# Optimization experiments

Hardware: AMD Instinct MI355X
Metric: run time of the kernel (lower is better)

## Reference

```python
import jax, jax.numpy as jnp
import numpy as np

B, S, D, H, E = 2, 2048, 1024, 4096, 8


def setup_inputs() -> dict:
    key = jax.random.key(0)
    ks = jax.random.split(key, 8)
    sc = lambda *shape: 0.02
    x = jax.random.normal(ks[0], (B, S, D), dtype=jnp.float32)
    gate_w = jax.random.normal(ks[1], (D, E), dtype=jnp.float32) * 0.02
    gate_b = jnp.zeros((E,), dtype=jnp.float32)
    w1 = jax.random.normal(ks[2], (E, D, H), dtype=jnp.float32) * 0.02
    b1 = jnp.zeros((E, H), dtype=jnp.float32)
    w2 = jax.random.normal(ks[3], (E, H, D), dtype=jnp.float32) * 0.02
    b2 = jnp.zeros((E, D), dtype=jnp.float32)
    return {"x": x, "gate_w": gate_w, "gate_b": gate_b,
            "w1": w1, "b1": b1, "w2": w2, "b2": b2}


def reference(x, gate_w, gate_b, w1, b1, w2, b2):
    b, s, d = x.shape
    e = w1.shape[0]
    xf = x.reshape(-1, d)                       # [N, D]
    scores = xf @ gate_w + gate_b               # [N, E]
    # original does topk(k=2) but only uses topk_indices[:, 0] == argmax
    sel = jnp.argmax(scores, axis=-1)           # [N]
    out = jnp.zeros_like(xf)
    for ei in range(e):                         # small fixed expert loop
        h = jax.nn.gelu(xf @ w1[ei] + b1[ei], approximate=False)
        y = h @ w2[ei] + b2[ei]
        out = out + jnp.where((sel == ei)[:, None], y, jnp.zeros((), x.dtype))
    out = out.reshape(b, s, d)
    l_aux = jnp.zeros((), dtype=x.dtype)
    return out, l_aux
```

## Files before the change

kernel.cpp:

```cpp
#include <hip/hip_runtime.h>
#include <math.h>

#define NTOK 4096
#define DDIM 1024
#define HDIM 4096
#define NEXP 8
#define BK 64
#define T0MAX 40
#define T1MAX 72
#define NG0 ((HDIM / 128) * T0MAX)
#define NCVT2 ((DDIM / 64) * (NEXP * (HDIM / 64)))

typedef float f32x4 __attribute__((ext_vector_type(4)));
typedef __bf16 bf16x8 __attribute__((ext_vector_type(8)));
typedef const __attribute__((address_space(1))) void gas_t;
typedef __attribute__((address_space(3))) void las_t;

__device__ __forceinline__ unsigned short f2bf(float f) {
    union { float f; unsigned u; } v; v.f = f;
    unsigned u = v.u;
    return (unsigned short)((u + 0x7fffu + ((u >> 16) & 1u)) >> 16);
}

__device__ __forceinline__ float gelu_f(float v) {
    return 0.5f * v * (1.0f + erff(v * 0.70710678118654752f));
}

__global__ void k_gate(const float* __restrict__ x, const float* __restrict__ gw,
                       const float* __restrict__ gb, unsigned short* __restrict__ xb,
                       int* __restrict__ sel, int* __restrict__ counts) {
    const int wid = threadIdx.x >> 6, lane = threadIdx.x & 63;
    const int tok = blockIdx.x * 4 + wid;
    const float4* xr4 = (const float4*)(x + (long)tok * DDIM);
    unsigned short* xbr = xb + (long)tok * DDIM;
    float s[NEXP];
#pragma unroll
    for (int e = 0; e < NEXP; ++e) s[e] = 0.f;
#pragma unroll
    for (int it = 0; it < DDIM / 256; ++it) {
        const int q = it * 64 + lane;
        const float4 xv = xr4[q];
        *(ushort4*)(xbr + q * 4) = make_ushort4(f2bf(xv.x), f2bf(xv.y), f2bf(xv.z), f2bf(xv.w));
#pragma unroll
        for (int j = 0; j < 4; ++j) {
            const float xs = (j == 0) ? xv.x : (j == 1) ? xv.y : (j == 2) ? xv.z : xv.w;
            const float4* g4 = (const float4*)(gw + (long)(q * 4 + j) * NEXP);
            const float4 g0 = g4[0], g1 = g4[1];
            s[0] += xs * g0.x; s[1] += xs * g0.y; s[2] += xs * g0.z; s[3] += xs * g0.w;
            s[4] += xs * g1.x; s[5] += xs * g1.y; s[6] += xs * g1.z; s[7] += xs * g1.w;
        }
    }
#pragma unroll
    for (int e = 0; e < NEXP; ++e)
        for (int off = 32; off > 0; off >>= 1)
            s[e] += __shfl_down(s[e], off);
    if (lane == 0) {
        float best = s[0] + gb[0]; int bi = 0;
#pragma unroll
        for (int e = 1; e < NEXP; ++e) {
            const float v = s[e] + gb[e];
            if (v > best) { best = v; bi = e; }
        }
        sel[tok] = bi;
        atomicAdd(&counts[bi], 1);
    }
}

__global__ void k_fill(const int* __restrict__ sel, const int* __restrict__ counts,
                       int* __restrict__ cur, int* __restrict__ offs,
                       int* __restrict__ list, int* __restrict__ t0,
                       int* __restrict__ t1, float* __restrict__ laux) {
    const int t = blockIdx.x * blockDim.x + threadIdx.x;
    if (t < NTOK) {
        const int e = sel[t];
        int off_e = 0;
#pragma unroll
        for (int j = 0; j < NEXP; ++j) off_e += (j < e) ? counts[j] : 0;
        list[off_e + atomicAdd(&cur[e], 1)] = t;
    }
    if (t == 0) {
        int o = 0;
        for (int e = 0; e < NEXP; ++e) { offs[e] = o; o += counts[e]; }
        offs[NEXP] = o;
        int i0 = 0;
        for (int e = 0; e < NEXP; ++e)
            for (int m = 0; m < counts[e]; m += 128) t0[i0++] = (e << 16) | m;
        while (i0 < T0MAX) t0[i0++] = -1;
        int i1 = 0;
        for (int e = 0; e < NEXP; ++e)
            for (int m = 0; m < counts[e]; m += 64) t1[i1++] = (e << 16) | m;
        while (i1 < T1MAX) t1[i1++] = -1;
        laux[0] = 0.f;
    }
}

template<int K, int NC>
__device__ __forceinline__ void cvt_tile(const float* __restrict__ W,
                                         unsigned short* __restrict__ Wt,
                                         int bx, int by, unsigned short* T) {
    constexpr int ktiles = K / 64;
    const int e  = by / ktiles;
    const int k0 = (by % ktiles) * 64;
    const int n0 = bx * 64;
    const float* src = W + (long)e * K * NC + (long)k0 * NC + n0;
    const int tid = threadIdx.x;
#pragma unroll
    for (int i = 0; i < 4; ++i) {
        const int idx = tid + i * 256;
        const int k = idx >> 4, c4 = (idx & 15) * 4;
        const float4 v = *(const float4*)(src + (long)k * NC + c4);
        T[(c4 + 0) * 68 + k] = f2bf(v.x);
        T[(c4 + 1) * 68 + k] = f2bf(v.y);
        T[(c4 + 2) * 68 + k] = f2bf(v.z);
        T[(c4 + 3) * 68 + k] = f2bf(v.w);
    }
    __syncthreads();
    unsigned short* dst = Wt + (long)e * NC * K + (long)n0 * K + k0;
#pragma unroll
    for (int i = 0; i < 2; ++i) {
        const int idx = tid + i * 256;
        const int n = idx >> 3, c8 = (idx & 7) * 8;
        *(ushort4*)(dst + (long)n * K + c8)     = *(const ushort4*)&T[n * 68 + c8];
        *(ushort4*)(dst + (long)n * K + c8 + 4) = *(const ushort4*)&T[n * 68 + c8 + 4];
    }
}

template<int K, int NC>
__global__ __launch_bounds__(256) void k_cvt_w(const float* __restrict__ W,
                                               unsigned short* __restrict__ Wt) {
    __shared__ unsigned short T[64 * 68];
    cvt_tile<K, NC>(W, Wt, blockIdx.x, blockIdx.y, T);
}

template<int MODE, int BM_, int BN_, bool FUSE>
__global__ __launch_bounds__(256) void k_gemm(
        const unsigned short* __restrict__ Ain,
        const unsigned short* __restrict__ Wt,
        const float* __restrict__ bias,
        unsigned short* __restrict__ Hout, float* __restrict__ Yout,
        const int* __restrict__ counts, const int* __restrict__ offs,
        const int* __restrict__ list, const int* __restrict__ ttab,
        const float* __restrict__ Wcvt, unsigned short* __restrict__ Wtcvt) {
    static_assert(BM_ % 32 == 0 && BN_ % 32 == 0, "tile");
    constexpr int K    = (MODE == 0) ? DDIM : HDIM;
    constexpr int NC   = (MODE == 0) ? HDIM : DDIM;
    constexpr int NT   = K / BK;
    constexpr int FM   = BM_ / 32;
    constexpr int FN   = BN_ / 32;
    constexpr int LA   = BM_ / 32;
    constexpr int LB   = BN_ / 32;
    constexpr int HALF = BM_ * 64 + BN_ * 64;
    constexpr int EP   = 136;
    constexpr int SH_SZ = (2 * HALF > BM_ * EP) ? 2 * HALF : BM_ * EP;

    __shared__ __align__(16) unsigned short sh[SH_SZ];

    int bx, by;
    if constexpr (FUSE) {
        const int bid = blockIdx.x;
        if (bid >= NG0) {
            const int cv = bid - NG0;
            cvt_tile<HDIM, DDIM>(Wcvt, Wtcvt, cv % (DDIM / 64), cv / (DDIM / 64), sh);
            return;
        }
        bx = bid % (NC / BN_); by = bid / (NC / BN_);
    } else {
        bx = blockIdx.x; by = blockIdx.y;
    }

    const int code = ttab[by];
    if (code < 0) return;
    const int e  = code >> 16;
    const int m0 = code & 0xFFFF;
    const int cnt  = counts[e];
    const int base = offs[e];
    const int n0   = bx * BN_;

    const int tid  = threadIdx.x;
    const int lane = tid & 63, wid = tid >> 6;
    const int lr = lane >> 3, lc = lane & 7;
    const int sb = (lc * 16) ^ (lr << 4);

    const unsigned short* pA[LA];
#pragma unroll
    for (int i = 0; i < LA; ++i) {
        const int r = wid * (BM_ / 4) + i * 8 + lr;
        int rr = m0 + r; if (rr >= cnt) rr = cnt - 1;
        const long grow = (MODE == 0) ? (long)list[base + rr] : (long)(base + rr);
        pA[i] = (const unsigned short*)((const char*)(Ain + grow * K) + sb);
    }
    const unsigned short* We = Wt + (long)e * NC * K;
    const unsigned short* pB[LB];
#pragma unroll
    for (int i = 0; i < LB; ++i) {
        const int r = wid * (BN_ / 4) + i * 8 + lr;
        pB[i] = (const unsigned short*)((const char*)(We + (long)(n0 + r) * K) + sb);
    }

    const int wm = (wid >> 1) * (BM_ / 2);
    const int wn = (wid & 1) * (BN_ / 2);
    const int hk = 16 * (lane >> 4);

#define STAGE(t) do { if ((t) < NT) {                                                    \
    unsigned short* Ad = sh + ((t) & 1) * HALF + (wid * (BM_ / 4)) * 64;                 \
    unsigned short* Bd = sh + ((t) & 1) * HALF + BM_ * 64 + (wid * (BN_ / 4)) * 64;      \
    _Pragma("unroll") for (int i = 0; i < LA; ++i)                                       \
        __builtin_amdgcn_global_load_lds((gas_t*)(pA[i] + (t) * 64),                     \
            (las_t*)(Ad + i * 512), 16, 0, 0);                                           \
    _Pragma("unroll") for (int i = 0; i < LB; ++i)                                       \
        __builtin_amdgcn_global_load_lds((gas_t*)(pB[i] + (t) * 64),                     \
            (las_t*)(Bd + i * 512), 16, 0, 0); } } while (0)

    const f32x4 zero4 = {0.f, 0.f, 0.f, 0.f};
    f32x4 acc[FM][FN];
#pragma unroll
    for (int i = 0; i < FM; ++i)
#pragma unroll
        for (int j = 0; j < FN; ++j) acc[i][j] = zero4;

    STAGE(0);
    STAGE(1);

    for (int t = 0; t < NT; ++t) {
        const unsigned short* Ab = sh + (t & 1) * HALF;
        const unsigned short* Bb = Ab + BM_ * 64;
        if (t + 1 < NT) { asm volatile("s_waitcnt vmcnt(%0)" :: "n"(LA + LB) : "memory"); }
        else            { asm volatile("s_waitcnt vmcnt(0)" ::: "memory"); }
        __builtin_amdgcn_sched_barrier(0);
        __builtin_amdgcn_s_barrier();
        __builtin_amdgcn_sched_barrier(0);
#pragma unroll
        for (int kk = 0; kk < BK; kk += 32) {
            bf16x8 a[FM], b[FN];
#pragma unroll
            for (int mf = 0; mf < FM; ++mf) {
                const int r  = wm + mf * 16 + (lane & 15);
                const int kb = (2 * kk + hk) ^ ((r & 7) << 4);
                a[mf] = *(const bf16x8*)((const char*)Ab + r * 128 + kb);
            }
#pragma unroll
            for (int nf = 0; nf < FN; ++nf) {
                const int cc = wn + nf * 16 + (lane & 15);
                const int kb = (2 * kk + hk) ^ ((cc & 7) << 4);
                b[nf] = *(const bf16x8*)((const char*)Bb + cc * 128 + kb);
            }
            __builtin_amdgcn_s_setprio(1);
#pragma unroll
            for (int mf = 0; mf < FM; ++mf)
#pragma unroll
                for (int nf = 0; nf < FN; ++nf)
                    acc[mf][nf] = __builtin_amdgcn_mfma_f32_16x16x32_bf16(
                        a[mf], b[nf], acc[mf][nf], 0, 0, 0);
            __builtin_amdgcn_s_setprio(0);
        }
        __builtin_amdgcn_sched_barrier(0);
        __builtin_amdgcn_s_barrier();
        __builtin_amdgcn_sched_barrier(0);
        STAGE(t + 2);
    }
#undef STAGE

    if constexpr (MODE == 0) {
#pragma unroll
        for (int nf = 0; nf < FN; ++nf) {
            const int cl = wn + nf * 16 + (lane & 15);
            const float bv = bias[(long)e * NC + n0 + cl];
#pragma unroll
            for (int mf = 0; mf < FM; ++mf) {
#pragma unroll
                for (int ri = 0; ri < 4; ++ri) {
                    const int rl = wm + mf * 16 + (lane >> 4) * 4 + ri;
                    sh[rl * EP + cl] = f2bf(gelu_f(acc[mf][nf][ri] + bv));
                }
            }
        }
        __syncthreads();
        const int row = tid >> 1, ch = (tid & 1) * 64;
        if (m0 + row < cnt) {
            char* dst = (char*)(Hout + (long)(base + m0 + row) * HDIM + n0 + ch);
            const char* srcp = (const char*)sh + row * (EP * 2) + ch * 2;
#pragma unroll
            for (int j = 0; j < 4; ++j) {
                const int4 v0 = *(const int4*)(srcp + j * 32);
                const int4 v1 = *(const int4*)(srcp + j * 32 + 16);
                *(int4*)(dst + j * 32)      = v0;
                *(int4*)(dst + j * 32 + 16) = v1;
            }
        }
    } else {
#pragma unroll
        for (int nf = 0; nf < FN; ++nf) {
            const int coln = n0 + wn + nf * 16 + (lane & 15);
            const float bv = bias[(long)e * NC + coln];
#pragma unroll
            for (int mf = 0; mf < FM; ++mf) {
                const int rb = m0 + wm + mf * 16 + (lane >> 4) * 4;
#pragma unroll
                for (int ri = 0; ri < 4; ++ri) {
                    const int row = rb + ri;
                    if (row < cnt)
                        Yout[(long)list[base + row] * DDIM + coln] = acc[mf][nf][ri] + bv;
                }
            }
        }
    }
}

extern "C" void kernel_launch(void* const* d_in, const int* in_sizes, int n_in,
                              void* d_out, int out_size, void* d_ws, size_t ws_size,
                              hipStream_t stream) {
    const float* x      = (const float*)d_in[0];
    const float* gate_w = (const float*)d_in[1];
    const float* gate_b = (const float*)d_in[2];
    const float* w1     = (const float*)d_in[3];
    const float* b1     = (const float*)d_in[4];
    const float* w2     = (const float*)d_in[5];
    const float* b2     = (const float*)d_in[6];
    float* out = (float*)d_out;

    char* ws = (char*)d_ws;
    int* counts  = (int*)(ws);
    int* cur     = (int*)(ws + 128);
    int* offs    = (int*)(ws + 256);
    int* t0      = (int*)(ws + 512);
    int* t1      = (int*)(ws + 768);
    int* sel     = (int*)(ws + 4096);
    int* list    = (int*)(ws + 20480);
    unsigned short* xb  = (unsigned short*)(ws + 65536);
    unsigned short* Hws = (unsigned short*)(ws + 65536 + 8388608);
    unsigned short* W1t = (unsigned short*)(ws + 65536 + 8388608 + 33554432);
    unsigned short* W2s = W1t + (size_t)NEXP * HDIM * DDIM;
    const size_t WS_SMALL = 65536 + 8388608 + 33554432 + 67108864;
    const size_t WS_BIG   = WS_SMALL + 67108864;
    if (ws_size < WS_SMALL) return;
    const bool big = ws_size >= WS_BIG;
    unsigned short* W2t = big ? W2s : W1t;

    hipMemsetAsync(ws, 0, 256, stream);
    k_gate<<<NTOK / 4, 256, 0, stream>>>(x, gate_w, gate_b, xb, sel, counts);
    k_fill<<<(NTOK + 255) / 256, 256, 0, stream>>>(sel, counts, cur, offs, list, t0, t1,
                                                   out + (long)NTOK * DDIM);

    k_cvt_w<DDIM, HDIM><<<dim3(HDIM / 64, NEXP * (DDIM / 64)), 256, 0, stream>>>(w1, W1t);

    if (big) {
        k_gemm<0, 128, 128, true><<<NG0 + NCVT2, 256, 0, stream>>>(
            xb, W1t, b1, Hws, nullptr, counts, offs, list, t0, w2, W2t);
    } else {
        k_gemm<0, 128, 128, false><<<dim3(HDIM / 128, T0MAX), 256, 0, stream>>>(
            xb, W1t, b1, Hws, nullptr, counts, offs, list, t0, nullptr, nullptr);
        k_cvt_w<HDIM, DDIM><<<dim3(DDIM / 64, NEXP * (HDIM / 64)), 256, 0, stream>>>(w2, W2t);
    }

    k_gemm<1, 64, 64, false><<<dim3(DDIM / 64, T1MAX), 256, 0, stream>>>(
        Hws, W2t, b2, nullptr, out, counts, offs, list, t1, nullptr, nullptr);
}
```

Before: 279.2 us.

## Fuse gate with W1 conversion, single-buffer GEMM staging, widen second GEMM tile

Folds the w1 fp32-to-bf16 transpose into the gating kernel as extra blocks, so one launch is removed and the conversion runs alongside gating. The GEMM's double-buffered async LDS prefetch is replaced by a single buffer with a load and two barriers every K step, which halves shared memory but stops global loads from overlapping with MFMA work. The second GEMM moves from 64x64 to 64x128 tiles, halving its grid. Exposed load latency in both GEMMs is the main risk.

```diff
diff --git a/kernel.cpp b/kernel.cpp
--- a/kernel.cpp
+++ b/kernel.cpp
@@ -8,7 +8,9 @@
 #define BK 64
 #define T0MAX 40
 #define T1MAX 72
-#define NG0 ((HDIM / 128) * T0MAX)
+#define NGATE (NTOK / 4)
+#define NCVT1 ((HDIM / 64) * (NEXP * (DDIM / 64)))
+#define NG0   ((HDIM / 128) * T0MAX)
 #define NCVT2 ((DDIM / 64) * (NEXP * (HDIM / 64)))
 
 typedef float f32x4 __attribute__((ext_vector_type(4)));
@@ -26,11 +28,51 @@
     return 0.5f * v * (1.0f + erff(v * 0.70710678118654752f));
 }
 
-__global__ void k_gate(const float* __restrict__ x, const float* __restrict__ gw,
-                       const float* __restrict__ gb, unsigned short* __restrict__ xb,
-                       int* __restrict__ sel, int* __restrict__ counts) {
+template<int K, int NC>
+__device__ __forceinline__ void cvt_tile(const float* __restrict__ W,
+                                         unsigned short* __restrict__ Wt,
+                                         int bx, int by, unsigned short* T) {
+    constexpr int ktiles = K / 64;
+    const int e  = by / ktiles;
+    const int k0 = (by % ktiles) * 64;
+    const int n0 = bx * 64;
+    const float* src = W + (long)e * K * NC + (long)k0 * NC + n0;
+    const int tid = threadIdx.x;
+#pragma unroll
+    for (int i = 0; i < 4; ++i) {
+        const int idx = tid + i * 256;
+        const int k = idx >> 4, c4 = (idx & 15) * 4;
+        const float4 v = *(const float4*)(src + (long)k * NC + c4);
+        T[(c4 + 0) * 68 + k] = f2bf(v.x);
+        T[(c4 + 1) * 68 + k] = f2bf(v.y);
+        T[(c4 + 2) * 68 + k] = f2bf(v.z);
+        T[(c4 + 3) * 68 + k] = f2bf(v.w);
+    }
+    __syncthreads();
+    unsigned short* dst = Wt + (long)e * NC * K + (long)n0 * K + k0;
+#pragma unroll
+    for (int i = 0; i < 2; ++i) {
+        const int idx = tid + i * 256;
+        const int n = idx >> 3, c8 = (idx & 7) * 8;
+        *(ushort4*)(dst + (long)n * K + c8)     = *(const ushort4*)&T[n * 68 + c8];
+        *(ushort4*)(dst + (long)n * K + c8 + 4) = *(const ushort4*)&T[n * 68 + c8 + 4];
+    }
+}
+
+__global__ __launch_bounds__(256) void k_gatecvt(
+        const float* __restrict__ x, const float* __restrict__ gw,
+        const float* __restrict__ gb, unsigned short* __restrict__ xb,
+        int* __restrict__ sel, int* __restrict__ counts,
+        const float* __restrict__ w1, unsigned short* __restrict__ W1t) {
+    __shared__ unsigned short T[64 * 68];
+    const int bid = blockIdx.x;
+    if (bid >= NGATE) {
+        const int cv = bid - NGATE;
+        cvt_tile<DDIM, HDIM>(w1, W1t, cv % (HDIM / 64), cv / (HDIM / 64), T);
+        return;
+    }
     const int wid = threadIdx.x >> 6, lane = threadIdx.x & 63;
-    const int tok = blockIdx.x * 4 + wid;
+    const int tok = bid * 4 + wid;
     const float4* xr4 = (const float4*)(x + (long)tok * DDIM);
     unsigned short* xbr = xb + (long)tok * DDIM;
     float s[NEXP];
@@ -91,37 +133,6 @@
             for (int m = 0; m < counts[e]; m += 64) t1[i1++] = (e << 16) | m;
         while (i1 < T1MAX) t1[i1++] = -1;
         laux[0] = 0.f;
-    }
-}
-
-template<int K, int NC>
-__device__ __forceinline__ void cvt_tile(const float* __restrict__ W,
-                                         unsigned short* __restrict__ Wt,
-                                         int bx, int by, unsigned short* T) {
-    constexpr int ktiles = K / 64;
-    const int e  = by / ktiles;
-    const int k0 = (by % ktiles) * 64;
-    const int n0 = bx * 64;
-    const float* src = W + (long)e * K * NC + (long)k0 * NC + n0;
-    const int tid = threadIdx.x;
-#pragma unroll
-    for (int i = 0; i < 4; ++i) {
-        const int idx = tid + i * 256;
-        const int k = idx >> 4, c4 = (idx & 15) * 4;
-        const float4 v = *(const float4*)(src + (long)k * NC + c4);
-        T[(c4 + 0) * 68 + k] = f2bf(v.x);
-        T[(c4 + 1) * 68 + k] = f2bf(v.y);
-        T[(c4 + 2) * 68 + k] = f2bf(v.z);
-        T[(c4 + 3) * 68 + k] = f2bf(v.w);
-    }
-    __syncthreads();
-    unsigned short* dst = Wt + (long)e * NC * K + (long)n0 * K + k0;
-#pragma unroll
-    for (int i = 0; i < 2; ++i) {
-        const int idx = tid + i * 256;
-        const int n = idx >> 3, c8 = (idx & 7) * 8;
-        *(ushort4*)(dst + (long)n * K + c8)     = *(const ushort4*)&T[n * 68 + c8];
-        *(ushort4*)(dst + (long)n * K + c8 + 4) = *(const ushort4*)&T[n * 68 + c8 + 4];
     }
 }
 
@@ -149,9 +160,9 @@
     constexpr int FN   = BN_ / 32;
     constexpr int LA   = BM_ / 32;
     constexpr int LB   = BN_ / 32;
-    constexpr int HALF = BM_ * 64 + BN_ * 64;
     constexpr int EP   = 136;
-    constexpr int SH_SZ = (2 * HALF > BM_ * EP) ? 2 * HALF : BM_ * EP;
+    constexpr int STAGE_SH = BM_ * 64 + BN_ * 64;
+    constexpr int SH_SZ = (MODE == 0 && BM_ * EP > STAGE_SH) ? BM_ * EP : STAGE_SH;
 
     __shared__ __align__(16) unsigned short sh[SH_SZ];
 
@@ -176,6 +187,9 @@
     const int base = offs[e];
     const int n0   = bx * BN_;
 
+    unsigned short* Asb = sh;
+    unsigned short* Btb = sh + BM_ * 64;
+
     const int tid  = threadIdx.x;
     const int lane = tid & 63, wid = tid >> 6;
     const int lr = lane >> 3, lc = lane & 7;
@@ -201,16 +215,6 @@
     const int wn = (wid & 1) * (BN_ / 2);
     const int hk = 16 * (lane >> 4);
 
-#define STAGE(t) do { if ((t) < NT) {                                                    \
-    unsigned short* Ad = sh + ((t) & 1) * HALF + (wid * (BM_ / 4)) * 64;                 \
-    unsigned short* Bd = sh + ((t) & 1) * HALF + BM_ * 64 + (wid * (BN_ / 4)) * 64;      \
-    _Pragma("unroll") for (int i = 0; i < LA; ++i)                                       \
-        __builtin_amdgcn_global_load_lds((gas_t*)(pA[i] + (t) * 64),                     \
-            (las_t*)(Ad + i * 512), 16, 0, 0);                                           \
-    _Pragma("unroll") for (int i = 0; i < LB; ++i)                                       \
-        __builtin_amdgcn_global_load_lds((gas_t*)(pB[i] + (t) * 64),                     \
-            (las_t*)(Bd + i * 512), 16, 0, 0); } } while (0)
-
     const f32x4 zero4 = {0.f, 0.f, 0.f, 0.f};
     f32x4 acc[FM][FN];
 #pragma unroll
@@ -218,17 +222,17 @@
 #pragma unroll
         for (int j = 0; j < FN; ++j) acc[i][j] = zero4;
 
-    STAGE(0);
-    STAGE(1);
-
     for (int t = 0; t < NT; ++t) {
-        const unsigned short* Ab = sh + (t & 1) * HALF;
-        const unsigned short* Bb = Ab + BM_ * 64;
-        if (t + 1 < NT) { asm volatile("s_waitcnt vmcnt(%0)" :: "n"(LA + LB) : "memory"); }
-        else            { asm volatile("s_waitcnt vmcnt(0)" ::: "memory"); }
-        __builtin_amdgcn_sched_barrier(0);
-        __builtin_amdgcn_s_barrier();
-        __builtin_amdgcn_sched_barrier(0);
+        __syncthreads();
+#pragma unroll
+        for (int i = 0; i < LA; ++i)
+            __builtin_amdgcn_global_load_lds((gas_t*)(pA[i] + t * 64),
+                (las_t*)(Asb + (wid * (BM_ / 4) + i * 8) * 64), 16, 0, 0);
+#pragma unroll
+        for (int i = 0; i < LB; ++i)
+            __builtin_amdgcn_global_load_lds((gas_t*)(pB[i] + t * 64),
+                (las_t*)(Btb + (wid * (BN_ / 4) + i * 8) * 64), 16, 0, 0);
+        __syncthreads();
 #pragma unroll
         for (int kk = 0; kk < BK; kk += 32) {
             bf16x8 a[FM], b[FN];
@@ -236,13 +240,13 @@
             for (int mf = 0; mf < FM; ++mf) {
                 const int r  = wm + mf * 16 + (lane & 15);
                 const int kb = (2 * kk + hk) ^ ((r & 7) << 4);
-                a[mf] = *(const bf16x8*)((const char*)Ab + r * 128 + kb);
+                a[mf] = *(const bf16x8*)((const char*)Asb + r * 128 + kb);
             }
 #pragma unroll
             for (int nf = 0; nf < FN; ++nf) {
                 const int cc = wn + nf * 16 + (lane & 15);
                 const int kb = (2 * kk + hk) ^ ((cc & 7) << 4);
-                b[nf] = *(const bf16x8*)((const char*)Bb + cc * 128 + kb);
+                b[nf] = *(const bf16x8*)((const char*)Btb + cc * 128 + kb);
             }
             __builtin_amdgcn_s_setprio(1);
 #pragma unroll
@@ -253,14 +257,10 @@
                         a[mf], b[nf], acc[mf][nf], 0, 0, 0);
             __builtin_amdgcn_s_setprio(0);
         }
-        __builtin_amdgcn_sched_barrier(0);
-        __builtin_amdgcn_s_barrier();
-        __builtin_amdgcn_sched_barrier(0);
-        STAGE(t + 2);
-    }
-#undef STAGE
+    }
 
     if constexpr (MODE == 0) {
+        __syncthreads();
 #pragma unroll
         for (int nf = 0; nf < FN; ++nf) {
             const int cl = wn + nf * 16 + (lane & 15);
@@ -337,11 +337,11 @@
     unsigned short* W2t = big ? W2s : W1t;
 
     hipMemsetAsync(ws, 0, 256, stream);
-    k_gate<<<NTOK / 4, 256, 0, stream>>>(x, gate_w, gate_b, xb, sel, counts);
+
+    k_gatecvt<<<NGATE + NCVT1, 256, 0, stream>>>(x, gate_w, gate_b, xb, sel, counts,
+                                                 w1, W1t);
     k_fill<<<(NTOK + 255) / 256, 256, 0, stream>>>(sel, counts, cur, offs, list, t0, t1,
                                                    out + (long)NTOK * DDIM);
-
-    k_cvt_w<DDIM, HDIM><<<dim3(HDIM / 64, NEXP * (DDIM / 64)), 256, 0, stream>>>(w1, W1t);
 
     if (big) {
         k_gemm<0, 128, 128, true><<<NG0 + NCVT2, 256, 0, stream>>>(
@@ -352,6 +352,6 @@
         k_cvt_w<HDIM, DDIM><<<dim3(DDIM / 64, NEXP * (HDIM / 64)), 256, 0, stream>>>(w2, W2t);
     }
 
-    k_gemm<1, 64, 64, false><<<dim3(DDIM / 64, T1MAX), 256, 0, stream>>>(
+    k_gemm<1, 64, 128, false><<<dim3(DDIM / 128, T1MAX), 256, 0, stream>>>(
         Hws, W2t, b2, nullptr, out, counts, offs, list, t1, nullptr, nullptr);
 }
```

After: 265.0 us. -5.1%, faster.
